# Kernel tuning notes

Measured on AMD Instinct MI355X. Metric: run time of the kernel, lower is better.

## Reference

```python
import jax, jax.numpy as jnp
import numpy as np

GROUPS = 8
EPS = 1e-5


def group_norm(x, gamma, beta):
    # x: (b, c, h, w); normalize per sample over each group of c//GROUPS channels and all spatial dims
    b, c, h, w = x.shape
    xg = x.reshape(b, GROUPS, c // GROUPS, h, w)
    mean = jnp.mean(xg, axis=(2, 3, 4), keepdims=True)
    var = jnp.var(xg, axis=(2, 3, 4), keepdims=True)
    xn = ((xg - mean) * jax.lax.rsqrt(var + EPS)).reshape(b, c, h, w)
    return xn * gamma[None, :, None, None] + beta[None, :, None, None]


def setup_inputs() -> dict:
    key = jax.random.key(0)
    k1, k2, k3 = jax.random.split(key, 3)
    b, c, h, w = 32, 256, 32, 32
    x = jax.random.normal(k1, (b, c, h, w), dtype=jnp.float32)
    qkv_w = jax.random.normal(k2, (3 * c, c), dtype=jnp.float32) * 0.02
    qkv_b = jnp.zeros((3 * c,), dtype=jnp.float32)
    out_w = jax.random.normal(k3, (c, c), dtype=jnp.float32) * 0.02
    out_b = jnp.zeros((c,), dtype=jnp.float32)
    gn_gamma = jnp.ones((c,), dtype=jnp.float32)
    gn_beta = jnp.zeros((c,), dtype=jnp.float32)
    return {"x": x, "gn_gamma": gn_gamma, "gn_beta": gn_beta,
            "qkv_w": qkv_w, "qkv_b": qkv_b, "out_w": out_w, "out_b": out_b}


def reference(x, gn_gamma, gn_beta, qkv_w, qkv_b, out_w, out_b):
    b, c, h, w = x.shape
    xn = group_norm(x, gn_gamma, gn_beta)
    # 1x1 conv == per-pixel linear: (b,c,h,w) x (3c,c) -> (b,3c,h,w)
    qkv = jnp.einsum('bchw,dc->bdhw', xn, qkv_w) + qkv_b[None, :, None, None]
    q, k, v = jnp.split(qkv, 3, axis=1)
    # (b, c, h, w) -> (b, hw, c)
    def tok(t):
        return t.transpose(0, 2, 3, 1).reshape(b, h * w, c)
    q, k, v = tok(q), tok(k), tok(v)
    scale = 1.0 / jnp.sqrt(jnp.asarray(c, dtype=x.dtype))
    scores = jnp.einsum('bnc,bmc->bnm', q, k) * scale  # (b, hw, hw)
    attn = jax.nn.softmax(scores, axis=-1)
    out = jnp.einsum('bnm,bmc->bnc', attn, v)  # (b, hw, c)
    out = out.reshape(b, h, w, c).transpose(0, 3, 1, 2)  # (b, c, h, w)
    out = jnp.einsum('bchw,dc->bdhw', out, out_w) + out_b[None, :, None, None]
    return out + x
```

## Files before the change

### kernel.cpp

```cpp
#include <hip/hip_runtime.h>
#include <hip/hip_bf16.h>
#include <stdint.h>


typedef __bf16 bf16_t;
typedef __bf16 bf16x4 __attribute__((ext_vector_type(4)));
typedef __bf16 bf16x8 __attribute__((ext_vector_type(8)));
typedef float f32x16 __attribute__((ext_vector_type(16)));
typedef _Float16 f16x4 __attribute__((ext_vector_type(4)));

#define MFMA32(a, b, c) __builtin_amdgcn_mfma_f32_32x32x16_bf16((a), (b), (c), 0, 0, 0)
#define GLL16(g, l)                                                                      \
    __builtin_amdgcn_global_load_lds((const __attribute__((address_space(1))) void*)(g), \
                                     (__attribute__((address_space(3))) void*)(l), 16, 0, 0)
#define WAITV8 asm volatile("s_waitcnt vmcnt(8)" ::: "memory")
#define WAITV0 asm volatile("s_waitcnt vmcnt(0)" ::: "memory")
#define WLG0   asm volatile("s_waitcnt lgkmcnt(0)" ::: "memory")
#define SBAR   __builtin_amdgcn_s_barrier()

#define QSCALE 0.0901684400555f

__device__ inline uint32_t pack2(float a, float b) {
    union { uint32_t u; __bf16 h[2]; } w;
    w.h[0] = (__bf16)a; w.h[1] = (__bf16)b;
    return w.u;
}

__global__ void cast_w(const float* __restrict__ s1, bf16_t* __restrict__ d1, int n1,
                       const float* __restrict__ s2, bf16_t* __restrict__ d2, int n2) {
    int i = blockIdx.x * blockDim.x + threadIdx.x;
    int stride = gridDim.x * blockDim.x;
    for (int k = i; k < n1; k += stride) d1[k] = (bf16_t)s1[k];
    for (int k = i; k < n2; k += stride) d2[k] = (bf16_t)s2[k];
}

__global__ __launch_bounds__(256) void gn_kernel(const float* __restrict__ x,
                                                 const float* __restrict__ gamma,
                                                 const float* __restrict__ beta,
                                                 bf16_t* __restrict__ xn) {
    extern __shared__ char gsm[];
    float* red = (float*)(gsm + 65536);
    int bg = blockIdx.x, b = bg >> 3, g = bg & 7;
    const float* base = x + (size_t)(b * 256 + g * 32) * 1024;
    int tid = threadIdx.x;

    float s = 0.f, ss = 0.f;
    #pragma unroll 4
    for (int c = 0; c < 32; c++) {
        float4 v = *(const float4*)(base + c * 1024 + tid * 4);
        s += v.x + v.y + v.z + v.w;
        ss += v.x * v.x + v.y * v.y + v.z * v.z + v.w * v.w;
        f16x4 h = {(_Float16)v.x, (_Float16)v.y, (_Float16)v.z, (_Float16)v.w};
        *(f16x4*)(gsm + c * 2048 + ((tid * 8) ^ ((c & 7) << 4))) = h;
    }
    for (int off = 32; off; off >>= 1) { s += __shfl_down(s, off); ss += __shfl_down(ss, off); }
    if ((tid & 63) == 0) { red[tid >> 6] = s; red[4 + (tid >> 6)] = ss; }
    __syncthreads();
    float S = red[0] + red[1] + red[2] + red[3];
    float SS = red[4] + red[5] + red[6] + red[7];
    float mean = S * (1.0f / 32768.0f);
    float var = SS * (1.0f / 32768.0f) - mean * mean;
    float rstd = rsqrtf(var + 1e-5f);

    int c = tid & 31;
    float gam = gamma[g * 32 + c] * rstd;
    float bet = beta[g * 32 + c] - mean * gam;
    bf16_t* dst = xn + (size_t)(b * 1024) * 256 + g * 32 + c;
    #pragma unroll 4
    for (int it = 0; it < 128; it++) {
        int p = it * 8 + (tid >> 5);
        _Float16 hv = *(_Float16*)(gsm + c * 2048 + ((p * 2) ^ ((c & 7) << 4)));
        dst[(size_t)p * 256] = (bf16_t)((float)hv * gam + bet);
    }
}

__global__ __launch_bounds__(256, 1) void gemm_qkv(const bf16_t* __restrict__ xn,
                                                   const bf16_t* __restrict__ wq,
                                                   const float* __restrict__ qkv_b,
                                                   bf16_t* __restrict__ qb,
                                                   bf16_t* __restrict__ kb,
                                                   bf16_t* __restrict__ vt) {
    extern __shared__ char smem[];
    char* As = smem;
    int tid = threadIdx.x, wv = tid >> 6, lane = tid & 63;
    int l31 = lane & 31, hi = lane >> 5;
    int t0 = blockIdx.x * 128;
    const char* asrc = (const char*)xn + (size_t)t0 * 512;
    const char* wsrc = (const char*)wq;

    {
        int u = lane & 31, rofs = lane >> 5;
        #pragma unroll
        for (int t = 0; t < 16; t++) {
            int r0 = t * 8 + wv * 2;
            int r = r0 + rofs;
            GLL16(asrc + (size_t)r * 512 + ((u ^ (r & 31)) * 16), As + r0 * 512);
        }
    }
    auto stage_B = [&](int nt) {
        char* Bd = smem + 65536 + (nt & 1) * 32768;
        int u = lane & 31, rofs = lane >> 5;
        #pragma unroll
        for (int t = 0; t < 8; t++) {
            int r0 = wv * 16 + t * 2;
            int r = r0 + rofs;
            GLL16(wsrc + (size_t)(nt * 64 + r) * 512 + ((u ^ (r & 31)) * 16), Bd + r0 * 512);
        }
    };
    stage_B(0);
    WAITV0; SBAR;

    int wm = wv >> 1, wd = wv & 1;
    int bb = t0 >> 10, pos0 = t0 & 1023;

    for (int nt = 0; nt < 12; nt++) {
        if (nt < 11) stage_B(nt + 1);
        const char* Bs = smem + 65536 + (nt & 1) * 32768;
        f32x16 acc0 = {}, acc1 = {};
        if (nt < 8) {
            __builtin_amdgcn_s_setprio(1);
            #pragma unroll
            for (int ks = 0; ks < 16; ks++) {
                int col = ks * 32 + hi * 16;
                bf16x8 a0 = *(const bf16x8*)(As + (wm * 64 + l31) * 512 + (col ^ (l31 << 4)));
                bf16x8 a1 = *(const bf16x8*)(As + (wm * 64 + 32 + l31) * 512 + (col ^ (l31 << 4)));
                bf16x8 b  = *(const bf16x8*)(Bs + (wd * 32 + l31) * 512 + (col ^ (l31 << 4)));
                acc0 = MFMA32(a0, b, acc0);
                acc1 = MFMA32(a1, b, acc1);
            }
            __builtin_amdgcn_s_setprio(0);
            int d = nt * 64 + wd * 32 + l31;
            bool isq = nt < 4;
            float bias = qkv_b[d];
            bf16_t* dst = isq ? qb : kb;
            int dd = isq ? d : d - 256;
            float sc = isq ? QSCALE : 1.0f;
            #pragma unroll
            for (int ms = 0; ms < 2; ms++) {
                #pragma unroll
                for (int r = 0; r < 16; r++) {
                    float v = ms ? acc1[r] : acc0[r];
                    int tok = t0 + wm * 64 + ms * 32 + (r & 3) + 8 * (r >> 2) + 4 * hi;
                    dst[(size_t)tok * 256 + dd] = (bf16_t)((v + bias) * sc);
                }
            }
        } else {
            __builtin_amdgcn_s_setprio(1);
            #pragma unroll
            for (int ks = 0; ks < 16; ks++) {
                int col = ks * 32 + hi * 16;
                bf16x8 a0 = *(const bf16x8*)(As + (wm * 64 + l31) * 512 + (col ^ (l31 << 4)));
                bf16x8 a1 = *(const bf16x8*)(As + (wm * 64 + 32 + l31) * 512 + (col ^ (l31 << 4)));
                bf16x8 b  = *(const bf16x8*)(Bs + (wd * 32 + l31) * 512 + (col ^ (l31 << 4)));
                acc0 = MFMA32(b, a0, acc0);
                acc1 = MFMA32(b, a1, acc1);
            }
            __builtin_amdgcn_s_setprio(0);
            int dbase = (nt - 8) * 64 + wd * 32;
            #pragma unroll
            for (int ms = 0; ms < 2; ms++) {
                int pos = pos0 + wm * 64 + ms * 32 + l31;
                #pragma unroll
                for (int r = 0; r < 16; r++) {
                    float v = ms ? acc1[r] : acc0[r];
                    int d = dbase + (r & 3) + 8 * (r >> 2) + 4 * hi;
                    vt[(size_t)bb * 262144 + (size_t)d * 1024 + pos] =
                        (bf16_t)(v + qkv_b[512 + d]);
                }
            }
        }
        if (nt < 11) { WAITV0; SBAR; }
    }
}

__global__ __launch_bounds__(256, 1) void attn_kernel(const bf16_t* __restrict__ qb,
                                                      const bf16_t* __restrict__ kb,
                                                      const bf16_t* __restrict__ vt,
                                                      bf16_t* __restrict__ ao) {
    extern __shared__ char smem[];
    int tid = threadIdx.x, i = blockIdx.x;
    int b = (i & 7) + ((i >> 6) << 3);
    int qt = (i >> 3) & 7;
    int wv = tid >> 6, lane = tid & 63, l31 = lane & 31, hi = lane >> 5;

    const char* kbase = (const char*)kb + (size_t)b * 524288;
    const char* vbase = (const char*)vt + (size_t)b * 524288;

    int qg = qt * 128 + wv * 32 + l31;
    const char* qsrc = (const char*)qb + (size_t)(b * 1024 + qg) * 512;
    bf16x8 qf[16];
    #pragma unroll
    for (int ks = 0; ks < 16; ks++) qf[ks] = *(const bf16x8*)(qsrc + ks * 32 + hi * 16);

    f32x16 o[8] = {};
    f32x16 sp0 = {}, sp1 = {};
    float mrun = -1e30f, lrun = 0.f;

    auto stage_K = [&](int ch) {
        char* Kd = smem + (ch & 1) * 32768;
        int j0 = ch * 64;
        #pragma unroll
        for (int t = 0; t < 8; t++) {
            int r0 = wv * 16 + t * 2;
            int r = r0 + (lane >> 5), u = lane & 31;
            GLL16(kbase + (size_t)(j0 + r) * 512 + ((u ^ (r & 31)) * 16), Kd + r0 * 512);
        }
    };
    auto stage_V = [&](int ch) {
        char* Vd = smem + 65536 + (ch & 1) * 32768;
        int j0 = ch * 64;
        #pragma unroll
        for (int t = 0; t < 8; t++) {
            int r0 = wv * 64 + t * 8;
            int r = r0 + (lane >> 3), u = lane & 7;
            int s5 = (((r & 3) << 3) | u) ^ ((r >> 2) & 31);
            int d_src = (r & ~3) | (s5 >> 3);
            GLL16(vbase + (size_t)d_src * 2048 + j0 * 2 + (s5 & 7) * 16, Vd + r0 * 128);
        }
    };
    auto qkt = [&](int ch, f32x16& s0, f32x16& s1) {
        const char* Ks = smem + (ch & 1) * 32768;
        __builtin_amdgcn_s_setprio(1);
        #pragma unroll
        for (int ks = 0; ks < 16; ks++) {
            int col = ks * 32 + hi * 16;
            bf16x8 k0 = *(const bf16x8*)(Ks + l31 * 512 + (col ^ (l31 << 4)));
            bf16x8 k1 = *(const bf16x8*)(Ks + (32 + l31) * 512 + (col ^ (l31 << 4)));
            s0 = MFMA32(k0, qf[ks], s0);
            s1 = MFMA32(k1, qf[ks], s1);
        }
        __builtin_amdgcn_s_setprio(0);
    };
    auto smax_pv = [&](f32x16& t0v, f32x16& t1v, int ch) {
        float mc = -1e30f;
        #pragma unroll
        for (int r = 0; r < 16; r++) mc = fmaxf(mc, fmaxf(t0v[r], t1v[r]));
        mc = fmaxf(mc, __shfl_xor(mc, 32));
        float mo = mrun;
        float mn = (mc <= mo + 8.0f) ? mo : mc;
        float rs = 0.f;
        #pragma unroll
        for (int r = 0; r < 16; r++) {
            t0v[r] = exp2f(t0v[r] - mn);
            t1v[r] = exp2f(t1v[r] - mn);
            rs += t0v[r] + t1v[r];
        }
        rs += __shfl_xor(rs, 32);
        float al = exp2f(mo - mn);
        lrun = lrun * al + rs;
        mrun = mn;
        if (__any(mn != mo)) {
            #pragma unroll
            for (int dt = 0; dt < 8; dt++) o[dt] = o[dt] * al;
        }
        const char* Vs = smem + 65536 + (ch & 1) * 32768;
        #pragma unroll
        for (int pk = 0; pk < 4; pk++) {
            float e0 = (pk < 2) ? t0v[(pk & 1) * 8 + 0] : t1v[(pk & 1) * 8 + 0];
            float e1 = (pk < 2) ? t0v[(pk & 1) * 8 + 1] : t1v[(pk & 1) * 8 + 1];
            float e2 = (pk < 2) ? t0v[(pk & 1) * 8 + 2] : t1v[(pk & 1) * 8 + 2];
            float e3 = (pk < 2) ? t0v[(pk & 1) * 8 + 3] : t1v[(pk & 1) * 8 + 3];
            float e4 = (pk < 2) ? t0v[(pk & 1) * 8 + 4] : t1v[(pk & 1) * 8 + 4];
            float e5 = (pk < 2) ? t0v[(pk & 1) * 8 + 5] : t1v[(pk & 1) * 8 + 5];
            float e6 = (pk < 2) ? t0v[(pk & 1) * 8 + 6] : t1v[(pk & 1) * 8 + 6];
            float e7 = (pk < 2) ? t0v[(pk & 1) * 8 + 7] : t1v[(pk & 1) * 8 + 7];
            uint32_t A0 = pack2(e0, e1), A1 = pack2(e2, e3);
            uint32_t B0 = pack2(e4, e5), B1 = pack2(e6, e7);
            asm volatile("v_permlane32_swap_b32 %0, %1" : "+v"(B0), "+v"(A0));
            asm volatile("v_permlane32_swap_b32 %0, %1" : "+v"(B1), "+v"(A1));
            union { bf16x8 v; uint32_t u[4]; } pw;
            pw.u[0] = A0; pw.u[1] = A1; pw.u[2] = B0; pw.u[3] = B1;
            __builtin_amdgcn_s_setprio(1);
            #pragma unroll
            for (int dt = 0; dt < 8; dt++) {
                int d = dt * 32 + l31;
                int a = (d * 128 + pk * 32 + hi * 16) ^ (((d >> 2) & 31) << 4);
                bf16x8 vf = *(const bf16x8*)(Vs + a);
                o[dt] = MFMA32(vf, pw.v, o[dt]);
            }
            __builtin_amdgcn_s_setprio(0);
        }
    };

    stage_K(0); stage_V(0);
    WAITV8; SBAR;
    stage_K(1);
    qkt(0, sp0, sp1);
    WLG0; SBAR;
    stage_V(1);

    for (int ch = 1; ch < 16; ch++) {
        WAITV8; SBAR;
        if (ch < 15) stage_K(ch + 1);
        f32x16 sn0 = {}, sn1 = {};
        qkt(ch, sn0, sn1);
        smax_pv(sp0, sp1, ch - 1);
        WLG0; SBAR;
        if (ch < 15) stage_V(ch + 1);
        sp0 = sn0; sp1 = sn1;
    }
    WAITV0; SBAR;
    smax_pv(sp0, sp1, 15);

    float inv = 1.0f / lrun;
    char* aod = (char*)ao + (size_t)(b * 1024 + qg) * 512;
    #pragma unroll
    for (int dt = 0; dt < 8; dt++) {
        #pragma unroll
        for (int rg = 0; rg < 4; rg++) {
            bf16x4 w;
            #pragma unroll
            for (int r = 0; r < 4; r++) w[r] = (bf16_t)(o[dt][rg * 4 + r] * inv);
            *(bf16x4*)(aod + dt * 64 + rg * 16 + hi * 8) = w;
        }
    }
}

__global__ __launch_bounds__(256, 1) void gemm_out(const bf16_t* __restrict__ wo,
                                                   const bf16_t* __restrict__ ao,
                                                   const float* __restrict__ out_b,
                                                   const float* __restrict__ x,
                                                   float* __restrict__ out) {
    extern __shared__ char smem[];
    char* Bs = smem;
    int tid = threadIdx.x, wv = tid >> 6, lane = tid & 63;
    int l31 = lane & 31, hi = lane >> 5;
    int t0 = blockIdx.x * 128;
    const char* bsrc = (const char*)ao + (size_t)t0 * 512;
    const char* wsrc = (const char*)wo;

    {
        int u = lane & 31, rofs = lane >> 5;
        #pragma unroll
        for (int t = 0; t < 16; t++) {
            int r0 = t * 8 + wv * 2;
            int r = r0 + rofs;
            GLL16(bsrc + (size_t)r * 512 + ((u ^ (r & 31)) * 16), Bs + r0 * 512);
        }
    }
    auto stage_W = [&](int ct) {
        char* Wd = smem + 65536 + (ct & 1) * 32768;
        int u = lane & 31, rofs = lane >> 5;
        #pragma unroll
        for (int t = 0; t < 8; t++) {
            int r0 = wv * 16 + t * 2;
            int r = r0 + rofs;
            GLL16(wsrc + (size_t)(ct * 64 + r) * 512 + ((u ^ (r & 31)) * 16), Wd + r0 * 512);
        }
    };
    stage_W(0);
    WAITV0; SBAR;

    int wm = wv >> 1, wc = wv & 1;
    int bb = t0 >> 10, pos0 = t0 & 1023;

    for (int ct = 0; ct < 4; ct++) {
        if (ct < 3) stage_W(ct + 1);
        const char* Ws = smem + 65536 + (ct & 1) * 32768;
        f32x16 acc0 = {}, acc1 = {};
        __builtin_amdgcn_s_setprio(1);
        #pragma unroll
        for (int ks = 0; ks < 16; ks++) {
            int col = ks * 32 + hi * 16;
            bf16x8 w  = *(const bf16x8*)(Ws + (wc * 32 + l31) * 512 + (col ^ (l31 << 4)));
            bf16x8 b0 = *(const bf16x8*)(Bs + (wm * 64 + l31) * 512 + (col ^ (l31 << 4)));
            bf16x8 b1 = *(const bf16x8*)(Bs + (wm * 64 + 32 + l31) * 512 + (col ^ (l31 << 4)));
            acc0 = MFMA32(w, b0, acc0);
            acc1 = MFMA32(w, b1, acc1);
        }
        __builtin_amdgcn_s_setprio(0);
        #pragma unroll
        for (int ms = 0; ms < 2; ms++) {
            int pos = pos0 + wm * 64 + ms * 32 + l31;
            #pragma unroll
            for (int r = 0; r < 16; r++) {
                float v = ms ? acc1[r] : acc0[r];
                int c = ct * 64 + wc * 32 + (r & 3) + 8 * (r >> 2) + 4 * hi;
                size_t idx = ((size_t)bb * 256 + c) * 1024 + pos;
                out[idx] = v + out_b[c] + x[idx];
            }
        }
        if (ct < 3) { WAITV0; SBAR; }
    }
}

extern "C" void kernel_launch(void* const* d_in, const int* in_sizes, int n_in,
                              void* d_out, int out_size, void* d_ws, size_t ws_size,
                              hipStream_t stream) {
    (void)in_sizes; (void)n_in; (void)out_size; (void)ws_size;
    const float* x      = (const float*)d_in[0];
    const float* gamma  = (const float*)d_in[1];
    const float* beta   = (const float*)d_in[2];
    const float* qkv_w  = (const float*)d_in[3];
    const float* qkv_b  = (const float*)d_in[4];
    const float* out_w  = (const float*)d_in[5];
    const float* out_b  = (const float*)d_in[6];
    float* out = (float*)d_out;

    char* ws = (char*)d_ws;
    const size_t MB16 = 16777216;
    bf16_t* xn  = (bf16_t*)(ws);
    bf16_t* qb  = (bf16_t*)(ws + 1 * MB16);
    bf16_t* kb  = (bf16_t*)(ws + 2 * MB16);
    bf16_t* vt  = (bf16_t*)(ws + 3 * MB16);
    bf16_t* ao  = (bf16_t*)(ws + 4 * MB16);
    bf16_t* wqb = (bf16_t*)(ws + 5 * MB16);
    bf16_t* wob = (bf16_t*)(ws + 5 * MB16 + 393216);

    cast_w<<<256, 256, 0, stream>>>(qkv_w, wqb, 196608, out_w, wob, 65536);
    gn_kernel<<<256, 256, 65600, stream>>>(x, gamma, beta, xn);
    gemm_qkv<<<256, 256, 131072, stream>>>(xn, wqb, qkv_b, qb, kb, vt);
    attn_kernel<<<256, 256, 131072, stream>>>(qb, kb, vt, ao);
    gemm_out<<<256, 256, 131072, stream>>>(wob, ao, out_b, x, out);
}
```

Before: 138.7 us.

## Split attention KV chunk across two wave groups with final softmax merge

The attention kernel now launches 512 threads per block, 8 waves instead of 4. Each query group of 32 rows is handled by two waves, and each of those waves processes half of every 64-key chunk, so per-wave QK^T and PV work is halved and there is more latency hiding per CU. At the end the two partial softmax states (o, m, l) are merged through shared memory. This adds an extra barrier and an LDS round-trip of 128 KB of fp32 accumulators. It also raises register pressure at 512 threads, and launch_bounds(512,2) cannot actually fit two blocks given the LDS size.

After: 220.1 us. 1.59x slower.

```diff
diff --git a/kernel.cpp b/kernel.cpp
--- a/kernel.cpp
+++ b/kernel.cpp
@@ -13,7 +13,7 @@
 #define GLL16(g, l)                                                                      \
     __builtin_amdgcn_global_load_lds((const __attribute__((address_space(1))) void*)(g), \
                                      (__attribute__((address_space(3))) void*)(l), 16, 0, 0)
-#define WAITV8 asm volatile("s_waitcnt vmcnt(8)" ::: "memory")
+#define WAITV4 asm volatile("s_waitcnt vmcnt(4)" ::: "memory")
 #define WAITV0 asm volatile("s_waitcnt vmcnt(0)" ::: "memory")
 #define WLG0   asm volatile("s_waitcnt lgkmcnt(0)" ::: "memory")
 #define SBAR   __builtin_amdgcn_s_barrier()
@@ -173,7 +173,7 @@
     }
 }
 
-__global__ __launch_bounds__(256, 1) void attn_kernel(const bf16_t* __restrict__ qb,
+__global__ __launch_bounds__(512, 2) void attn_kernel(const bf16_t* __restrict__ qb,
                                                       const bf16_t* __restrict__ kb,
                                                       const bf16_t* __restrict__ vt,
                                                       bf16_t* __restrict__ ao) {
@@ -182,26 +182,27 @@
     int b = (i & 7) + ((i >> 6) << 3);
     int qt = (i >> 3) & 7;
     int wv = tid >> 6, lane = tid & 63, l31 = lane & 31, hi = lane >> 5;
+    int qgrp = wv & 3, kh = wv >> 2;
 
     const char* kbase = (const char*)kb + (size_t)b * 524288;
     const char* vbase = (const char*)vt + (size_t)b * 524288;
 
-    int qg = qt * 128 + wv * 32 + l31;
+    int qg = qt * 128 + qgrp * 32 + l31;
     const char* qsrc = (const char*)qb + (size_t)(b * 1024 + qg) * 512;
     bf16x8 qf[16];
     #pragma unroll
     for (int ks = 0; ks < 16; ks++) qf[ks] = *(const bf16x8*)(qsrc + ks * 32 + hi * 16);
 
     f32x16 o[8] = {};
-    f32x16 sp0 = {}, sp1 = {};
+    f32x16 sp = {};
     float mrun = -1e30f, lrun = 0.f;
 
     auto stage_K = [&](int ch) {
         char* Kd = smem + (ch & 1) * 32768;
         int j0 = ch * 64;
         #pragma unroll
-        for (int t = 0; t < 8; t++) {
-            int r0 = wv * 16 + t * 2;
+        for (int t = 0; t < 4; t++) {
+            int r0 = wv * 8 + t * 2;
             int r = r0 + (lane >> 5), u = lane & 31;
             GLL16(kbase + (size_t)(j0 + r) * 512 + ((u ^ (r & 31)) * 16), Kd + r0 * 512);
         }
@@ -210,40 +211,38 @@
         char* Vd = smem + 65536 + (ch & 1) * 32768;
         int j0 = ch * 64;
         #pragma unroll
-        for (int t = 0; t < 8; t++) {
-            int r0 = wv * 64 + t * 8;
+        for (int t = 0; t < 4; t++) {
+            int r0 = wv * 32 + t * 8;
             int r = r0 + (lane >> 3), u = lane & 7;
             int s5 = (((r & 3) << 3) | u) ^ ((r >> 2) & 31);
             int d_src = (r & ~3) | (s5 >> 3);
             GLL16(vbase + (size_t)d_src * 2048 + j0 * 2 + (s5 & 7) * 16, Vd + r0 * 128);
         }
     };
-    auto qkt = [&](int ch, f32x16& s0, f32x16& s1) {
+    auto qkt = [&](int ch, f32x16& s0) {
         const char* Ks = smem + (ch & 1) * 32768;
+        int krow = kh * 32 + l31;
         __builtin_amdgcn_s_setprio(1);
         #pragma unroll
         for (int ks = 0; ks < 16; ks++) {
             int col = ks * 32 + hi * 16;
-            bf16x8 k0 = *(const bf16x8*)(Ks + l31 * 512 + (col ^ (l31 << 4)));
-            bf16x8 k1 = *(const bf16x8*)(Ks + (32 + l31) * 512 + (col ^ (l31 << 4)));
+            bf16x8 k0 = *(const bf16x8*)(Ks + krow * 512 + (col ^ (l31 << 4)));
             s0 = MFMA32(k0, qf[ks], s0);
-            s1 = MFMA32(k1, qf[ks], s1);
         }
         __builtin_amdgcn_s_setprio(0);
     };
-    auto smax_pv = [&](f32x16& t0v, f32x16& t1v, int ch) {
+    auto smax_pv = [&](f32x16& sv, int ch) {
         float mc = -1e30f;
         #pragma unroll
-        for (int r = 0; r < 16; r++) mc = fmaxf(mc, fmaxf(t0v[r], t1v[r]));
+        for (int r = 0; r < 16; r++) mc = fmaxf(mc, sv[r]);
         mc = fmaxf(mc, __shfl_xor(mc, 32));
         float mo = mrun;
         float mn = (mc <= mo + 8.0f) ? mo : mc;
         float rs = 0.f;
         #pragma unroll
         for (int r = 0; r < 16; r++) {
-            t0v[r] = exp2f(t0v[r] - mn);
-            t1v[r] = exp2f(t1v[r] - mn);
-            rs += t0v[r] + t1v[r];
+            sv[r] = exp2f(sv[r] - mn);
+            rs += sv[r];
         }
         rs += __shfl_xor(rs, 32);
         float al = exp2f(mo - mn);
@@ -255,15 +254,11 @@
         }
         const char* Vs = smem + 65536 + (ch & 1) * 32768;
         #pragma unroll
-        for (int pk = 0; pk < 4; pk++) {
-            float e0 = (pk < 2) ? t0v[(pk & 1) * 8 + 0] : t1v[(pk & 1) * 8 + 0];
-            float e1 = (pk < 2) ? t0v[(pk & 1) * 8 + 1] : t1v[(pk & 1) * 8 + 1];
-            float e2 = (pk < 2) ? t0v[(pk & 1) * 8 + 2] : t1v[(pk & 1) * 8 + 2];
-            float e3 = (pk < 2) ? t0v[(pk & 1) * 8 + 3] : t1v[(pk & 1) * 8 + 3];
-            float e4 = (pk < 2) ? t0v[(pk & 1) * 8 + 4] : t1v[(pk & 1) * 8 + 4];
-            float e5 = (pk < 2) ? t0v[(pk & 1) * 8 + 5] : t1v[(pk & 1) * 8 + 5];
-            float e6 = (pk < 2) ? t0v[(pk & 1) * 8 + 6] : t1v[(pk & 1) * 8 + 6];
-            float e7 = (pk < 2) ? t0v[(pk & 1) * 8 + 7] : t1v[(pk & 1) * 8 + 7];
+        for (int pk = 0; pk < 2; pk++) {
+            float e0 = sv[pk * 8 + 0], e1 = sv[pk * 8 + 1];
+            float e2 = sv[pk * 8 + 2], e3 = sv[pk * 8 + 3];
+            float e4 = sv[pk * 8 + 4], e5 = sv[pk * 8 + 5];
+            float e6 = sv[pk * 8 + 6], e7 = sv[pk * 8 + 7];
             uint32_t A0 = pack2(e0, e1), A1 = pack2(e2, e3);
             uint32_t B0 = pack2(e4, e5), B1 = pack2(e6, e7);
             asm volatile("v_permlane32_swap_b32 %0, %1" : "+v"(B0), "+v"(A0));
@@ -274,7 +269,7 @@
             #pragma unroll
             for (int dt = 0; dt < 8; dt++) {
                 int d = dt * 32 + l31;
-                int a = (d * 128 + pk * 32 + hi * 16) ^ (((d >> 2) & 31) << 4);
+                int a = (d * 128 + kh * 64 + pk * 32 + hi * 16) ^ (((d >> 2) & 31) << 4);
                 bf16x8 vf = *(const bf16x8*)(Vs + a);
                 o[dt] = MFMA32(vf, pw.v, o[dt]);
             }
@@ -283,35 +278,56 @@
     };
 
     stage_K(0); stage_V(0);
-    WAITV8; SBAR;
+    WAITV4; SBAR;
     stage_K(1);
-    qkt(0, sp0, sp1);
+    qkt(0, sp);
     WLG0; SBAR;
     stage_V(1);
 
     for (int ch = 1; ch < 16; ch++) {
-        WAITV8; SBAR;
+        WAITV4; SBAR;
         if (ch < 15) stage_K(ch + 1);
-        f32x16 sn0 = {}, sn1 = {};
-        qkt(ch, sn0, sn1);
-        smax_pv(sp0, sp1, ch - 1);
+        f32x16 sn = {};
+        qkt(ch, sn);
+        smax_pv(sp, ch - 1);
         WLG0; SBAR;
         if (ch < 15) stage_V(ch + 1);
-        sp0 = sn0; sp1 = sn1;
+        sp = sn;
     }
     WAITV0; SBAR;
-    smax_pv(sp0, sp1, 15);
-
-    float inv = 1.0f / lrun;
-    char* aod = (char*)ao + (size_t)(b * 1024 + qg) * 512;
-    #pragma unroll
-    for (int dt = 0; dt < 8; dt++) {
-        #pragma unroll
-        for (int rg = 0; rg < 4; rg++) {
-            bf16x4 w;
-            #pragma unroll
-            for (int r = 0; r < 4; r++) w[r] = (bf16_t)(o[dt][rg * 4 + r] * inv);
-            *(bf16x4*)(aod + dt * 64 + rg * 16 + hi * 8) = w;
+    smax_pv(sp, 15);
+
+    __syncthreads();
+    float* mlb = (float*)(smem + 131072);
+    if (kh == 1) {
+        char* dst = smem + qgrp * 32768 + lane * 512;
+        #pragma unroll
+        for (int dt = 0; dt < 8; dt++) *(f32x16*)(dst + dt * 64) = o[dt];
+        mlb[(qgrp * 64 + lane) * 2] = mrun;
+        mlb[(qgrp * 64 + lane) * 2 + 1] = lrun;
+    }
+    __syncthreads();
+    if (kh == 0) {
+        float m1 = mlb[(qgrp * 64 + lane) * 2];
+        float l1 = mlb[(qgrp * 64 + lane) * 2 + 1];
+        float mm = fmaxf(mrun, m1);
+        float a0 = exp2f(mrun - mm), a1 = exp2f(m1 - mm);
+        float linv = 1.0f / (lrun * a0 + l1 * a1);
+        const char* srcp = smem + qgrp * 32768 + lane * 512;
+        char* aod = (char*)ao + (size_t)(b * 1024 + qg) * 512;
+        #pragma unroll
+        for (int dt = 0; dt < 8; dt++) {
+            f32x16 o1 = *(const f32x16*)(srcp + dt * 64);
+            #pragma unroll
+            for (int rg = 0; rg < 4; rg++) {
+                bf16x4 w;
+                #pragma unroll
+                for (int r = 0; r < 4; r++) {
+                    float v = (o[dt][rg * 4 + r] * a0 + o1[rg * 4 + r] * a1) * linv;
+                    w[r] = (bf16_t)v;
+                }
+                *(bf16x4*)(aod + dt * 64 + rg * 16 + hi * 8) = w;
+            }
         }
     }
 }
@@ -410,6 +426,6 @@
     cast_w<<<256, 256, 0, stream>>>(qkv_w, wqb, 196608, out_w, wob, 65536);
     gn_kernel<<<256, 256, 65600, stream>>>(x, gamma, beta, xn);
     gemm_qkv<<<256, 256, 131072, stream>>>(xn, wqb, qkv_b, qb, kb, vt);
-    attn_kernel<<<256, 256, 131072, stream>>>(qb, kb, vt, ao);
+    attn_kernel<<<256, 512, 133120, stream>>>(qb, kb, vt, ao);
     gemm_out<<<256, 256, 131072, stream>>>(wob, ao, out_b, x, out);
 }
```

## Split attention head dim across 8 waves with 3-stage KV ring buffer

Applied to the files above, without the earlier changes.

The attention kernel goes from 4 to 8 waves per block. Each pair of waves shares a 32-query group and splits the 256-wide output head dimension in half, so each wave holds 4 instead of 8 output accumulators. K/V staging becomes one triple-buffered 32-key chunk per iteration, loaded jointly, replacing the separate double-buffered 64-key K and V pipeline with its QK/softmax software overlap. This means QK^T scores are computed redundantly by both waves of a pair, and each chunk gets more barriers, in exchange for lower register pressure and more waves to hide latency.

New measurement: 139.2 us. Within noise of the previous version (+0.4%).

```diff
diff --git a/kernel.cpp b/kernel.cpp
--- a/kernel.cpp
+++ b/kernel.cpp
@@ -13,9 +13,8 @@
 #define GLL16(g, l)                                                                      \
     __builtin_amdgcn_global_load_lds((const __attribute__((address_space(1))) void*)(g), \
                                      (__attribute__((address_space(3))) void*)(l), 16, 0, 0)
-#define WAITV8 asm volatile("s_waitcnt vmcnt(8)" ::: "memory")
+#define WAITV4 asm volatile("s_waitcnt vmcnt(4)" ::: "memory")
 #define WAITV0 asm volatile("s_waitcnt vmcnt(0)" ::: "memory")
-#define WLG0   asm volatile("s_waitcnt lgkmcnt(0)" ::: "memory")
 #define SBAR   __builtin_amdgcn_s_barrier()
 
 #define QSCALE 0.0901684400555f
@@ -173,7 +172,7 @@
     }
 }
 
-__global__ __launch_bounds__(256, 1) void attn_kernel(const bf16_t* __restrict__ qb,
+__global__ __launch_bounds__(512, 1) void attn_kernel(const bf16_t* __restrict__ qb,
                                                       const bf16_t* __restrict__ kb,
                                                       const bf16_t* __restrict__ vt,
                                                       bf16_t* __restrict__ ao) {
@@ -182,68 +181,69 @@
     int b = (i & 7) + ((i >> 6) << 3);
     int qt = (i >> 3) & 7;
     int wv = tid >> 6, lane = tid & 63, l31 = lane & 31, hi = lane >> 5;
+    int qgrp = wv & 3, dh = wv >> 2;
 
     const char* kbase = (const char*)kb + (size_t)b * 524288;
     const char* vbase = (const char*)vt + (size_t)b * 524288;
 
-    int qg = qt * 128 + wv * 32 + l31;
+    int qg = qt * 128 + qgrp * 32 + l31;
     const char* qsrc = (const char*)qb + (size_t)(b * 1024 + qg) * 512;
     bf16x8 qf[16];
     #pragma unroll
     for (int ks = 0; ks < 16; ks++) qf[ks] = *(const bf16x8*)(qsrc + ks * 32 + hi * 16);
 
-    f32x16 o[8] = {};
-    f32x16 sp0 = {}, sp1 = {};
+    f32x16 o[4] = {};
     float mrun = -1e30f, lrun = 0.f;
 
-    auto stage_K = [&](int ch) {
-        char* Kd = smem + (ch & 1) * 32768;
-        int j0 = ch * 64;
-        #pragma unroll
-        for (int t = 0; t < 8; t++) {
-            int r0 = wv * 16 + t * 2;
-            int r = r0 + (lane >> 5), u = lane & 31;
-            GLL16(kbase + (size_t)(j0 + r) * 512 + ((u ^ (r & 31)) * 16), Kd + r0 * 512);
+    auto stage = [&](int ch) {
+        char* Kd = smem + (ch % 3) * 32768;
+        char* Vd = Kd + 16384;
+        int j0 = ch * 32;
+        #pragma unroll
+        for (int p = 0; p < 2; p++) {
+            int Ls = (tid << 4) + (p << 13);
+            int s = Ls ^ (((Ls >> 9) & 31) << 4);
+            int dstoff = wv * 1024 + p * 8192;
+            GLL16(kbase + (size_t)(j0 + (Ls >> 9)) * 512 + (s & 511), Kd + dstoff);
+            GLL16(vbase + (size_t)(s >> 6) * 2048 + j0 * 2 + (s & 63), Vd + dstoff);
         }
     };
-    auto stage_V = [&](int ch) {
-        char* Vd = smem + 65536 + (ch & 1) * 32768;
-        int j0 = ch * 64;
-        #pragma unroll
-        for (int t = 0; t < 8; t++) {
-            int r0 = wv * 64 + t * 8;
-            int r = r0 + (lane >> 3), u = lane & 7;
-            int s5 = (((r & 3) << 3) | u) ^ ((r >> 2) & 31);
-            int d_src = (r & ~3) | (s5 >> 3);
-            GLL16(vbase + (size_t)d_src * 2048 + j0 * 2 + (s5 & 7) * 16, Vd + r0 * 128);
-        }
-    };
-    auto qkt = [&](int ch, f32x16& s0, f32x16& s1) {
-        const char* Ks = smem + (ch & 1) * 32768;
+
+    stage(0);
+    stage(1);
+
+    for (int ch = 0; ch < 32; ch++) {
+        if (ch < 31) { WAITV4; } else { WAITV0; }
+        SBAR;
+        if (ch + 2 < 32) stage(ch + 2);
+        const char* Ks = smem + (ch % 3) * 32768;
+        const char* Vs = Ks + 16384;
+
+        f32x16 se = {}, so2 = {};
         __builtin_amdgcn_s_setprio(1);
         #pragma unroll
-        for (int ks = 0; ks < 16; ks++) {
-            int col = ks * 32 + hi * 16;
-            bf16x8 k0 = *(const bf16x8*)(Ks + l31 * 512 + (col ^ (l31 << 4)));
-            bf16x8 k1 = *(const bf16x8*)(Ks + (32 + l31) * 512 + (col ^ (l31 << 4)));
-            s0 = MFMA32(k0, qf[ks], s0);
-            s1 = MFMA32(k1, qf[ks], s1);
+        for (int ks = 0; ks < 16; ks += 2) {
+            int c0 = ks * 32 + hi * 16;
+            int c1 = c0 + 32;
+            bf16x8 k0 = *(const bf16x8*)(Ks + l31 * 512 + (c0 ^ (l31 << 4)));
+            bf16x8 k1 = *(const bf16x8*)(Ks + l31 * 512 + (c1 ^ (l31 << 4)));
+            se = MFMA32(k0, qf[ks], se);
+            so2 = MFMA32(k1, qf[ks + 1], so2);
         }
         __builtin_amdgcn_s_setprio(0);
-    };
-    auto smax_pv = [&](f32x16& t0v, f32x16& t1v, int ch) {
+        f32x16 sv = se + so2;
+
         float mc = -1e30f;
         #pragma unroll
-        for (int r = 0; r < 16; r++) mc = fmaxf(mc, fmaxf(t0v[r], t1v[r]));
+        for (int r = 0; r < 16; r++) mc = fmaxf(mc, sv[r]);
         mc = fmaxf(mc, __shfl_xor(mc, 32));
         float mo = mrun;
         float mn = (mc <= mo + 8.0f) ? mo : mc;
         float rs = 0.f;
         #pragma unroll
         for (int r = 0; r < 16; r++) {
-            t0v[r] = exp2f(t0v[r] - mn);
-            t1v[r] = exp2f(t1v[r] - mn);
-            rs += t0v[r] + t1v[r];
+            sv[r] = exp2f(sv[r] - mn);
+            rs += sv[r];
         }
         rs += __shfl_xor(rs, 32);
         float al = exp2f(mo - mn);
@@ -251,61 +251,35 @@
         mrun = mn;
         if (__any(mn != mo)) {
             #pragma unroll
-            for (int dt = 0; dt < 8; dt++) o[dt] = o[dt] * al;
-        }
-        const char* Vs = smem + 65536 + (ch & 1) * 32768;
-        #pragma unroll
-        for (int pk = 0; pk < 4; pk++) {
-            float e0 = (pk < 2) ? t0v[(pk & 1) * 8 + 0] : t1v[(pk & 1) * 8 + 0];
-            float e1 = (pk < 2) ? t0v[(pk & 1) * 8 + 1] : t1v[(pk & 1) * 8 + 1];
-            float e2 = (pk < 2) ? t0v[(pk & 1) * 8 + 2] : t1v[(pk & 1) * 8 + 2];
-            float e3 = (pk < 2) ? t0v[(pk & 1) * 8 + 3] : t1v[(pk & 1) * 8 + 3];
-            float e4 = (pk < 2) ? t0v[(pk & 1) * 8 + 4] : t1v[(pk & 1) * 8 + 4];
-            float e5 = (pk < 2) ? t0v[(pk & 1) * 8 + 5] : t1v[(pk & 1) * 8 + 5];
-            float e6 = (pk < 2) ? t0v[(pk & 1) * 8 + 6] : t1v[(pk & 1) * 8 + 6];
-            float e7 = (pk < 2) ? t0v[(pk & 1) * 8 + 7] : t1v[(pk & 1) * 8 + 7];
-            uint32_t A0 = pack2(e0, e1), A1 = pack2(e2, e3);
-            uint32_t B0 = pack2(e4, e5), B1 = pack2(e6, e7);
+            for (int dt = 0; dt < 4; dt++) o[dt] = o[dt] * al;
+        }
+
+        #pragma unroll
+        for (int pk = 0; pk < 2; pk++) {
+            uint32_t A0 = pack2(sv[pk * 8 + 0], sv[pk * 8 + 1]);
+            uint32_t A1 = pack2(sv[pk * 8 + 2], sv[pk * 8 + 3]);
+            uint32_t B0 = pack2(sv[pk * 8 + 4], sv[pk * 8 + 5]);
+            uint32_t B1 = pack2(sv[pk * 8 + 6], sv[pk * 8 + 7]);
             asm volatile("v_permlane32_swap_b32 %0, %1" : "+v"(B0), "+v"(A0));
             asm volatile("v_permlane32_swap_b32 %0, %1" : "+v"(B1), "+v"(A1));
             union { bf16x8 v; uint32_t u[4]; } pw;
             pw.u[0] = A0; pw.u[1] = A1; pw.u[2] = B0; pw.u[3] = B1;
             __builtin_amdgcn_s_setprio(1);
             #pragma unroll
-            for (int dt = 0; dt < 8; dt++) {
-                int d = dt * 32 + l31;
-                int a = (d * 128 + pk * 32 + hi * 16) ^ (((d >> 2) & 31) << 4);
+            for (int dt = 0; dt < 4; dt++) {
+                int d = dh * 128 + dt * 32 + l31;
+                int a = (d * 64 + pk * 32 + hi * 16) ^ (((d >> 3) & 31) << 4);
                 bf16x8 vf = *(const bf16x8*)(Vs + a);
                 o[dt] = MFMA32(vf, pw.v, o[dt]);
             }
             __builtin_amdgcn_s_setprio(0);
         }
-    };
-
-    stage_K(0); stage_V(0);
-    WAITV8; SBAR;
-    stage_K(1);
-    qkt(0, sp0, sp1);
-    WLG0; SBAR;
-    stage_V(1);
-
-    for (int ch = 1; ch < 16; ch++) {
-        WAITV8; SBAR;
-        if (ch < 15) stage_K(ch + 1);
-        f32x16 sn0 = {}, sn1 = {};
-        qkt(ch, sn0, sn1);
-        smax_pv(sp0, sp1, ch - 1);
-        WLG0; SBAR;
-        if (ch < 15) stage_V(ch + 1);
-        sp0 = sn0; sp1 = sn1;
-    }
-    WAITV0; SBAR;
-    smax_pv(sp0, sp1, 15);
+    }
 
     float inv = 1.0f / lrun;
-    char* aod = (char*)ao + (size_t)(b * 1024 + qg) * 512;
+    char* aod = (char*)ao + (size_t)(b * 1024 + qg) * 512 + dh * 256;
     #pragma unroll
-    for (int dt = 0; dt < 8; dt++) {
+    for (int dt = 0; dt < 4; dt++) {
         #pragma unroll
         for (int rg = 0; rg < 4; rg++) {
             bf16x4 w;
@@ -410,6 +384,6 @@
     cast_w<<<256, 256, 0, stream>>>(qkv_w, wqb, 196608, out_w, wob, 65536);
     gn_kernel<<<256, 256, 65600, stream>>>(x, gamma, beta, xn);
     gemm_qkv<<<256, 256, 131072, stream>>>(xn, wqb, qkv_b, qb, kb, vt);
-    attn_kernel<<<256, 256, 131072, stream>>>(qb, kb, vt, ao);
+    attn_kernel<<<256, 512, 98304, stream>>>(qb, kb, vt, ao);
     gemm_out<<<256, 256, 131072, stream>>>(wob, ao, out_b, x, out);
 }
```

## Replace skewed QK/PV software pipeline with simple double-buffered attention loop

Applied to the files above, without the earlier changes.

Removes the skewed schedule, which overlapped QK^T for chunk ch with softmax and PV for chunk ch-1 and staged K and V separately under fine-grained vmcnt waits. Each iteration now issues K and V loads for the next chunk, then runs QK^T, softmax and PV on the current chunk, and ends with a __syncthreads. The V tile in LDS is re-laid out as two 64-byte-wide halves with a new XOR swizzle, and the setprio hints are dropped. The loop is simpler and needs fewer live score registers, but MFMA work inside a wave is no longer interleaved across chunks, and the full barrier each iteration may expose load latency.

After: 139.2 us. About the same (+0.3%).

```diff
diff --git a/kernel.cpp b/kernel.cpp
--- a/kernel.cpp
+++ b/kernel.cpp
@@ -13,9 +13,7 @@
 #define GLL16(g, l)                                                                      \
     __builtin_amdgcn_global_load_lds((const __attribute__((address_space(1))) void*)(g), \
                                      (__attribute__((address_space(3))) void*)(l), 16, 0, 0)
-#define WAITV8 asm volatile("s_waitcnt vmcnt(8)" ::: "memory")
 #define WAITV0 asm volatile("s_waitcnt vmcnt(0)" ::: "memory")
-#define WLG0   asm volatile("s_waitcnt lgkmcnt(0)" ::: "memory")
 #define SBAR   __builtin_amdgcn_s_barrier()
 
 #define QSCALE 0.0901684400555f
@@ -193,11 +191,11 @@
     for (int ks = 0; ks < 16; ks++) qf[ks] = *(const bf16x8*)(qsrc + ks * 32 + hi * 16);
 
     f32x16 o[8] = {};
-    f32x16 sp0 = {}, sp1 = {};
     float mrun = -1e30f, lrun = 0.f;
 
-    auto stage_K = [&](int ch) {
+    auto stage = [&](int ch) {
         char* Kd = smem + (ch & 1) * 32768;
+        char* Vd = smem + 65536 + (ch & 1) * 32768;
         int j0 = ch * 64;
         #pragma unroll
         for (int t = 0; t < 8; t++) {
@@ -205,45 +203,48 @@
             int r = r0 + (lane >> 5), u = lane & 31;
             GLL16(kbase + (size_t)(j0 + r) * 512 + ((u ^ (r & 31)) * 16), Kd + r0 * 512);
         }
+        #pragma unroll
+        for (int h = 0; h < 2; h++) {
+            #pragma unroll
+            for (int p = 0; p < 4; p++) {
+                int Ls = (tid << 4) + (p << 12);
+                int s = Ls ^ (((Ls >> 9) & 31) << 4);
+                GLL16(vbase + (size_t)(s >> 6) * 2048 + j0 * 2 + h * 64 + (s & 63),
+                      Vd + h * 16384 + (p << 12) + wv * 1024);
+            }
+        }
     };
-    auto stage_V = [&](int ch) {
-        char* Vd = smem + 65536 + (ch & 1) * 32768;
-        int j0 = ch * 64;
-        #pragma unroll
-        for (int t = 0; t < 8; t++) {
-            int r0 = wv * 64 + t * 8;
-            int r = r0 + (lane >> 3), u = lane & 7;
-            int s5 = (((r & 3) << 3) | u) ^ ((r >> 2) & 31);
-            int d_src = (r & ~3) | (s5 >> 3);
-            GLL16(vbase + (size_t)d_src * 2048 + j0 * 2 + (s5 & 7) * 16, Vd + r0 * 128);
-        }
-    };
-    auto qkt = [&](int ch, f32x16& s0, f32x16& s1) {
+
+    stage(0);
+    __syncthreads();
+
+    for (int ch = 0; ch < 16; ch++) {
         const char* Ks = smem + (ch & 1) * 32768;
-        __builtin_amdgcn_s_setprio(1);
+        const char* Vs = smem + 65536 + (ch & 1) * 32768;
+        if (ch < 15) stage(ch + 1);
+
+        f32x16 sv0 = {}, sv1 = {};
         #pragma unroll
         for (int ks = 0; ks < 16; ks++) {
             int col = ks * 32 + hi * 16;
             bf16x8 k0 = *(const bf16x8*)(Ks + l31 * 512 + (col ^ (l31 << 4)));
             bf16x8 k1 = *(const bf16x8*)(Ks + (32 + l31) * 512 + (col ^ (l31 << 4)));
-            s0 = MFMA32(k0, qf[ks], s0);
-            s1 = MFMA32(k1, qf[ks], s1);
-        }
-        __builtin_amdgcn_s_setprio(0);
-    };
-    auto smax_pv = [&](f32x16& t0v, f32x16& t1v, int ch) {
+            sv0 = MFMA32(k0, qf[ks], sv0);
+            sv1 = MFMA32(k1, qf[ks], sv1);
+        }
+
         float mc = -1e30f;
         #pragma unroll
-        for (int r = 0; r < 16; r++) mc = fmaxf(mc, fmaxf(t0v[r], t1v[r]));
+        for (int r = 0; r < 16; r++) mc = fmaxf(mc, fmaxf(sv0[r], sv1[r]));
         mc = fmaxf(mc, __shfl_xor(mc, 32));
         float mo = mrun;
         float mn = (mc <= mo + 8.0f) ? mo : mc;
         float rs = 0.f;
         #pragma unroll
         for (int r = 0; r < 16; r++) {
-            t0v[r] = exp2f(t0v[r] - mn);
-            t1v[r] = exp2f(t1v[r] - mn);
-            rs += t0v[r] + t1v[r];
+            sv0[r] = exp2f(sv0[r] - mn);
+            sv1[r] = exp2f(sv1[r] - mn);
+            rs += sv0[r] + sv1[r];
         }
         rs += __shfl_xor(rs, 32);
         float al = exp2f(mo - mn);
@@ -253,54 +254,34 @@
             #pragma unroll
             for (int dt = 0; dt < 8; dt++) o[dt] = o[dt] * al;
         }
-        const char* Vs = smem + 65536 + (ch & 1) * 32768;
+
         #pragma unroll
         for (int pk = 0; pk < 4; pk++) {
-            float e0 = (pk < 2) ? t0v[(pk & 1) * 8 + 0] : t1v[(pk & 1) * 8 + 0];
-            float e1 = (pk < 2) ? t0v[(pk & 1) * 8 + 1] : t1v[(pk & 1) * 8 + 1];
-            float e2 = (pk < 2) ? t0v[(pk & 1) * 8 + 2] : t1v[(pk & 1) * 8 + 2];
-            float e3 = (pk < 2) ? t0v[(pk & 1) * 8 + 3] : t1v[(pk & 1) * 8 + 3];
-            float e4 = (pk < 2) ? t0v[(pk & 1) * 8 + 4] : t1v[(pk & 1) * 8 + 4];
-            float e5 = (pk < 2) ? t0v[(pk & 1) * 8 + 5] : t1v[(pk & 1) * 8 + 5];
-            float e6 = (pk < 2) ? t0v[(pk & 1) * 8 + 6] : t1v[(pk & 1) * 8 + 6];
-            float e7 = (pk < 2) ? t0v[(pk & 1) * 8 + 7] : t1v[(pk & 1) * 8 + 7];
+            float e0 = (pk < 2) ? sv0[(pk & 1) * 8 + 0] : sv1[(pk & 1) * 8 + 0];
+            float e1 = (pk < 2) ? sv0[(pk & 1) * 8 + 1] : sv1[(pk & 1) * 8 + 1];
+            float e2 = (pk < 2) ? sv0[(pk & 1) * 8 + 2] : sv1[(pk & 1) * 8 + 2];
+            float e3 = (pk < 2) ? sv0[(pk & 1) * 8 + 3] : sv1[(pk & 1) * 8 + 3];
+            float e4 = (pk < 2) ? sv0[(pk & 1) * 8 + 4] : sv1[(pk & 1) * 8 + 4];
+            float e5 = (pk < 2) ? sv0[(pk & 1) * 8 + 5] : sv1[(pk & 1) * 8 + 5];
+            float e6 = (pk < 2) ? sv0[(pk & 1) * 8 + 6] : sv1[(pk & 1) * 8 + 6];
+            float e7 = (pk < 2) ? sv0[(pk & 1) * 8 + 7] : sv1[(pk & 1) * 8 + 7];
             uint32_t A0 = pack2(e0, e1), A1 = pack2(e2, e3);
             uint32_t B0 = pack2(e4, e5), B1 = pack2(e6, e7);
             asm volatile("v_permlane32_swap_b32 %0, %1" : "+v"(B0), "+v"(A0));
             asm volatile("v_permlane32_swap_b32 %0, %1" : "+v"(B1), "+v"(A1));
             union { bf16x8 v; uint32_t u[4]; } pw;
             pw.u[0] = A0; pw.u[1] = A1; pw.u[2] = B0; pw.u[3] = B1;
-            __builtin_amdgcn_s_setprio(1);
+            const char* Vh = Vs + (pk >> 1) * 16384;
             #pragma unroll
             for (int dt = 0; dt < 8; dt++) {
                 int d = dt * 32 + l31;
-                int a = (d * 128 + pk * 32 + hi * 16) ^ (((d >> 2) & 31) << 4);
-                bf16x8 vf = *(const bf16x8*)(Vs + a);
+                int a = (d * 64 + (pk & 1) * 32 + hi * 16) ^ (((d >> 3) & 31) << 4);
+                bf16x8 vf = *(const bf16x8*)(Vh + a);
                 o[dt] = MFMA32(vf, pw.v, o[dt]);
             }
-            __builtin_amdgcn_s_setprio(0);
-        }
-    };
-
-    stage_K(0); stage_V(0);
-    WAITV8; SBAR;
-    stage_K(1);
-    qkt(0, sp0, sp1);
-    WLG0; SBAR;
-    stage_V(1);
-
-    for (int ch = 1; ch < 16; ch++) {
-        WAITV8; SBAR;
-        if (ch < 15) stage_K(ch + 1);
-        f32x16 sn0 = {}, sn1 = {};
-        qkt(ch, sn0, sn1);
-        smax_pv(sp0, sp1, ch - 1);
-        WLG0; SBAR;
-        if (ch < 15) stage_V(ch + 1);
-        sp0 = sn0; sp1 = sn1;
-    }
-    WAITV0; SBAR;
-    smax_pv(sp0, sp1, 15);
+        }
+        __syncthreads();
+    }
 
     float inv = 1.0f / lrun;
     char* aod = (char*)ao + (size_t)(b * 1024 + qg) * 512;
```
